# Kernel optimization log

Hardware: AMD Instinct MI355X
Metric: run time of the kernel (lower is better)

The kernel has to match this reference:

```python
import jax, jax.numpy as jnp
import numpy as np

N_NODES = 100000
N_EDGES = 3200000
N_GRAPHS = 2048
VOCAB = 92
H = 64
N_LAYERS = 3


def setup_inputs() -> dict:
    key = jax.random.key(0)
    ks = jax.random.split(key, 16)
    x = jax.random.randint(ks[0], (N_NODES,), 0, VOCAB)
    edge_index = jax.random.randint(ks[1], (2, N_EDGES), 0, N_NODES)
    batch = jnp.sort(jax.random.randint(ks[2], (N_NODES,), 0, N_GRAPHS))
    s = 0.1
    return {
        "x": x,
        "edge_index": edge_index,
        "batch": batch,
        "emb": jax.random.normal(ks[3], (VOCAB, H), jnp.float32) * s,
        "conv_w": jax.random.normal(ks[4], (N_LAYERS, H, H), jnp.float32) * s,
        "conv_b": jax.random.normal(ks[5], (N_LAYERS, H), jnp.float32) * s,
        "w1": jax.random.normal(ks[6], (H, H // 2), jnp.float32) * s,
        "b1": jax.random.normal(ks[7], (H // 2,), jnp.float32) * s,
        "w2": jax.random.normal(ks[8], (H // 2, H // 4), jnp.float32) * s,
        "b2": jax.random.normal(ks[9], (H // 4,), jnp.float32) * s,
        "w3": jax.random.normal(ks[10], (H // 4, 1), jnp.float32) * s,
        "b3": jax.random.normal(ks[11], (1,), jnp.float32) * s,
    }


def _gcn_graph(edge_index, n_nodes):
    # add self-loops, then symmetric degree normalization (PyG GCNConv default)
    loop = jnp.arange(n_nodes)
    row = jnp.concatenate([edge_index[0], loop])  # source
    col = jnp.concatenate([edge_index[1], loop])  # target (aggregation index)
    deg = jnp.zeros((n_nodes,), jnp.float32).at[col].add(1.0)
    dinv = jnp.where(deg > 0, jax.lax.rsqrt(deg), 0.0)
    norm = dinv[row] * dinv[col]  # [E+N]
    return row, col, norm


def _forward(x, edge_index, batch, emb, conv_w, conv_b, w1, b1, w2, b2, w3, b3):
    n = x.shape[0]
    row, col, norm = _gcn_graph(edge_index, n)
    h = emb[x]  # [N,H] embedding lookup
    for i in range(N_LAYERS):
        t = h @ conv_w[i]  # linear transform first (GCNConv)
        msg = t[row] * norm[:, None]  # gather + edge scaling
        agg = jax.ops.segment_sum(msg, col, num_segments=n)  # scatter-add
        h_new = jax.nn.relu(agg + conv_b[i])
        h = h_new if i == 0 else h + h_new  # residual after first layer
    # global mean pool over graphs
    sums = jax.ops.segment_sum(h, batch, num_segments=N_GRAPHS)
    cnt = jax.ops.segment_sum(jnp.ones((n,), h.dtype), batch, num_segments=N_GRAPHS)
    g = sums / jnp.maximum(cnt, 1.0)[:, None]  # [G,H]
    # predictor MLP (dropout is identity in eval)
    g = jax.nn.relu(g @ w1 + b1)
    g = jax.nn.relu(g @ w2 + b2)
    return g @ w3 + b3  # [G,1]


def reference(x, edge_index, batch, emb, conv_w, conv_b, w1, b1, w2, b2, w3, b3):
    return _forward(x, edge_index, batch, emb, conv_w, conv_b, w1, b1, w2, b2, w3, b3)
```

## Files before the change

kernel.cpp:

```cpp
#include <hip/hip_runtime.h>

#define N_NODES 100000
#define N_EDGES 3200000
#define N_GRAPHS 2048
#define VOCAB 92
#define H 64
#define N_LAYERS 3

#define BUCK_BITS 6
#define BUCK_NODES (1 << BUCK_BITS)
#define NBUCK ((N_NODES + BUCK_NODES - 1) / BUCK_NODES)

#define PART_BLOCKS 256
#define EDGES_PER_PART (N_EDGES / PART_BLOCKS)
#define BS_STRIDE (NBUCK + 1)

#define BIN_CAP 2560

#define G0_TILE 64
#define SBINS_STRIDE 100
#define SB_STRIDE 104

#define FL_TILE 64
#define A_STRIDE 72

typedef _Float16 half8 __attribute__((ext_vector_type(8)));
typedef _Float16 half2t __attribute__((ext_vector_type(2)));
typedef float f32x4 __attribute__((ext_vector_type(4)));

__device__ inline unsigned short f2bf(float f) {
    union { float f; unsigned u; } v; v.f = f;
    unsigned u = v.u;
    u += 0x7fffu + ((u >> 16) & 1u);
    return (unsigned short)(u >> 16);
}
__device__ inline float bfhi(unsigned p) {
    union { unsigned u; float f; } v; v.u = p & 0xffff0000u; return v.f;
}
__device__ inline float bflo(unsigned p) {
    union { unsigned u; float f; } v; v.u = p << 16; return v.f;
}
__device__ inline float bf2f(unsigned short b) {
    union { unsigned u; float f; } v; v.u = ((unsigned)b) << 16; return v.f;
}


__device__ inline unsigned char fp8e(float v) {
    union { float f; unsigned u; } a; a.f = v + 0.015625f;
    unsigned u = a.u + 0x0007FFFFu + ((a.u >> 20) & 1u);
    return (unsigned char)((u >> 20) - 960u);
}

__device__ inline half2t ph(unsigned u) {
    union { unsigned u; half2t h; } t; t.u = u; return t.h;
}
__device__ inline unsigned hu(half2t h) {
    union { half2t h; unsigned u; } t; t.h = h; return t.u;
}

__device__ inline void unpack_add8(uint2 v, half2t* a) {
    a[0] += ph(((v.x & 0x00FF00FFu) << 7) + 0x20002000u);
    a[1] += ph(((v.x >> 1) & 0x7F807F80u) + 0x20002000u);
    a[2] += ph(((v.y & 0x00FF00FFu) << 7) + 0x20002000u);
    a[3] += ph(((v.y >> 1) & 0x7F807F80u) + 0x20002000u);
}


__global__ void k_pre(const float* __restrict__ emb, const float* __restrict__ W0,
                      float* __restrict__ M, int* __restrict__ bcnt,
                      int* __restrict__ srpad) {
    int v = blockIdx.x, c = threadIdx.x;
    int i = v * 64 + c;
    if (i < NBUCK) bcnt[i] = 0;
    if (v == 0 && c < 64) srpad[c] = 0;
    float acc = 0.0f;
#pragma unroll
    for (int k = 0; k < H; ++k) acc += emb[v * H + k] * W0[k * H + c];
    M[v * H + c] = acc;
}

__global__ __launch_bounds__(1024) void k_binA(const int* __restrict__ row,
                                               const int* __restrict__ col,
                                               int* __restrict__ bcnt,
                                               int* __restrict__ blkstart,
                                               int* __restrict__ staging) {
    __shared__ int lh[NBUCK];
    __shared__ int lsc[NBUCK];
    __shared__ int s[2048];
    int tid = threadIdx.x;
    int base = blockIdx.x * EDGES_PER_PART;

    for (int i = tid; i < NBUCK; i += 1024) lh[i] = 0;
    __syncthreads();
    for (int k = tid; k < EDGES_PER_PART; k += 1024)
        atomicAdd(&lh[col[base + k] >> BUCK_BITS], 1);
    __syncthreads();

    int p0 = tid, p1 = tid + 1024;
    int v0 = (p0 < NBUCK) ? lh[p0] : 0;
    int v1 = (p1 < NBUCK) ? lh[p1] : 0;
    s[p0] = v0; s[p1] = v1;
    __syncthreads();
    for (int off = 1; off < 2048; off <<= 1) {
        int t0 = (p0 >= off) ? s[p0 - off] : 0;
        int t1 = (p1 >= off) ? s[p1 - off] : 0;
        __syncthreads();
        s[p0] += t0; s[p1] += t1;
        __syncthreads();
    }
    int* myrow = blkstart + (size_t)blockIdx.x * BS_STRIDE;
    if (p0 < NBUCK) {
        int e = s[p0] - v0;
        lsc[p0] = e;
        myrow[p0] = base + e;
        if (v0) atomicAdd(&bcnt[p0], v0);
        lh[p0] = 0;
    }
    if (p1 < NBUCK) {
        int e = s[p1] - v1;
        lsc[p1] = e;
        myrow[p1] = base + e;
        if (v1) atomicAdd(&bcnt[p1], v1);
        lh[p1] = 0;
    }
    if (tid == 0) myrow[NBUCK] = base + EDGES_PER_PART;
    __syncthreads();

    for (int k = tid; k < EDGES_PER_PART; k += 1024) {
        int c = col[base + k];
        int b = c >> BUCK_BITS;
        int r = atomicAdd(&lh[b], 1);
        staging[base + lsc[b] + r] = row[base + k] | ((c & (BUCK_NODES - 1)) << 17);
    }
}

__global__ void k_bscan(const int* __restrict__ bcnt, int* __restrict__ bbase) {
    __shared__ int s[2048];
    int tid = threadIdx.x;
    int p0 = tid, p1 = tid + 1024;
    int v0 = (p0 < NBUCK) ? bcnt[p0] : 0;
    int v1 = (p1 < NBUCK) ? bcnt[p1] : 0;
    s[p0] = v0; s[p1] = v1;
    __syncthreads();
    for (int off = 1; off < 2048; off <<= 1) {
        int t0 = (p0 >= off) ? s[p0 - off] : 0;
        int t1 = (p1 >= off) ? s[p1 - off] : 0;
        __syncthreads();
        s[p0] += t0; s[p1] += t1;
        __syncthreads();
    }
    if (p0 < NBUCK) bbase[p0] = s[p0] - v0;
    if (p1 < NBUCK) bbase[p1] = s[p1] - v1;
    if (tid == 0) bbase[NBUCK] = N_EDGES;
}

__global__ __launch_bounds__(256) void k_binB(const int* __restrict__ staging,
                                              const int* __restrict__ blkstart,
                                              const int* __restrict__ bbase,
                                              const int* __restrict__ x,
                                              int* __restrict__ sorted_e,
                                              int* __restrict__ degi,
                                              int* __restrict__ row_start,
                                              float* __restrict__ dinv,
                                              unsigned* __restrict__ packed) {
    __shared__ int lde[BUCK_NODES];
    __shared__ int lsc[BUCK_NODES];
    __shared__ int sl[BIN_CAP];
    __shared__ int s2[PART_BLOCKS];
    int b = blockIdx.x, tid = threadIdx.x;
    int n0 = b << BUCK_BITS;
    int s0 = bbase[b], s1 = bbase[b + 1];
    int total = s1 - s0;
    bool fit = (total <= BIN_CAP);

    const int* brow = blkstart + (size_t)tid * BS_STRIDE;
    int st = brow[b];
    int cnt = brow[b + 1] - st;

    if (tid < BUCK_NODES) lde[tid] = 0;
    s2[tid] = cnt;
    __syncthreads();
    for (int off = 1; off < PART_BLOCKS; off <<= 1) {
        int v = (tid >= off) ? s2[tid - off] : 0;
        __syncthreads();
        s2[tid] += v;
        __syncthreads();
    }
    int excl = s2[tid] - cnt;

    if (fit) {
        for (int i = 0; i < cnt; ++i) {
            int p = staging[st + i];
            sl[excl + i] = p;
            atomicAdd(&lde[p >> 17], 1);
        }
    } else {
        for (int i = 0; i < cnt; ++i)
            atomicAdd(&lde[staging[st + i] >> 17], 1);
    }
    __syncthreads();

    if (tid < BUCK_NODES) lsc[tid] = lde[tid];
    __syncthreads();
    for (int off = 1; off < BUCK_NODES; off <<= 1) {
        int v = (tid >= off && tid < BUCK_NODES) ? lsc[tid - off] : 0;
        __syncthreads();
        if (tid < BUCK_NODES) lsc[tid] += v;
        __syncthreads();
    }
    if (tid < BUCK_NODES) {
        int n = n0 + tid;
        int ex = lsc[tid] - lde[tid];
        if (n < N_NODES) {
            row_start[n] = s0 + ex;
            degi[n] = lde[tid];
            float dv = rsqrtf((float)(lde[tid] + 1));
            dinv[n] = dv;
            packed[n] = ((unsigned)f2bf(dv) << 16) | (unsigned)x[n];
        }
        lsc[tid] = ex;
        lde[tid] = 0;
    }
    __syncthreads();
    if (fit) {
        for (int i = tid; i < total; i += 256) {
            int p = sl[i];
            int ln = p >> 17;
            int r = atomicAdd(&lde[ln], 1);
            sorted_e[s0 + lsc[ln] + r] = p;
        }
    } else {
        for (int i = 0; i < cnt; ++i) {
            int p = staging[st + i];
            int ln = p >> 17;
            int r = atomicAdd(&lde[ln], 1);
            sorted_e[s0 + lsc[ln] + r] = p;
        }
    }
}

__global__ __launch_bounds__(256) void k_gather0_mfma(
    const int* __restrict__ sorted_e, const int* __restrict__ bbase,
    const unsigned* __restrict__ packed,
    const float* __restrict__ M, const float* __restrict__ dinv,
    const float* __restrict__ bias, unsigned short* __restrict__ h,
    unsigned char* __restrict__ qout) {
    __shared__ float Sbins[G0_TILE][SBINS_STRIDE];
    __shared__ _Float16 Sb[G0_TILE][SB_STRIDE];
    __shared__ _Float16 Blds[H][SB_STRIDE];

    int tid = threadIdx.x;
    int b = blockIdx.x;
    int n0 = b << BUCK_BITS;

    for (int i = tid; i < G0_TILE * SBINS_STRIDE; i += 256)
        ((float*)Sbins)[i] = 0.0f;
    {
        int c = tid & 63, v0 = tid >> 6;
        for (int v = v0; v < VOCAB; v += 4)
            Blds[c][v] = (_Float16)M[v * H + c];
        Blds[c][VOCAB + v0] = (_Float16)0.0f;
    }
    __syncthreads();

    if (tid < G0_TILE) {
        int n = n0 + tid;
        if (n < N_NODES) {
            unsigned p = packed[n];
            atomicAdd(&Sbins[tid][p & 127u], __uint_as_float(p & 0xffff0000u));
        }
    }
    {
        int s0 = bbase[b], s1 = bbase[b + 1];
        int i = s0 + tid;
        for (; i + 256 < s1; i += 512) {
            int p0 = sorted_e[i];
            int p1 = sorted_e[i + 256];
            unsigned k0 = packed[p0 & 0x1FFFF];
            unsigned k1 = packed[p1 & 0x1FFFF];
            atomicAdd(&Sbins[p0 >> 17][k0 & 127u], __uint_as_float(k0 & 0xffff0000u));
            atomicAdd(&Sbins[p1 >> 17][k1 & 127u], __uint_as_float(k1 & 0xffff0000u));
        }
        if (i < s1) {
            int p0 = sorted_e[i];
            unsigned k0 = packed[p0 & 0x1FFFF];
            atomicAdd(&Sbins[p0 >> 17][k0 & 127u], __uint_as_float(k0 & 0xffff0000u));
        }
    }
    __syncthreads();

    {
        int r0 = tid >> 2, k0 = (tid & 3) * 24;
#pragma unroll
        for (int m = 0; m < 3; ++m) {
            f32x4 f0 = *(const f32x4*)&Sbins[r0][k0 + 8 * m];
            f32x4 f1 = *(const f32x4*)&Sbins[r0][k0 + 8 * m + 4];
            half8 o;
            o[0] = (_Float16)f0[0]; o[1] = (_Float16)f0[1];
            o[2] = (_Float16)f0[2]; o[3] = (_Float16)f0[3];
            o[4] = (_Float16)f1[0]; o[5] = (_Float16)f1[1];
            o[6] = (_Float16)f1[2]; o[7] = (_Float16)f1[3];
            *(half8*)&Sb[r0][k0 + 8 * m] = o;
        }
    }
    __syncthreads();

    int w = tid >> 6, lane = tid & 63;
    int l15 = lane & 15, l4 = lane >> 4;
    half8 afr[3];
#pragma unroll
    for (int ks = 0; ks < 3; ++ks)
        afr[ks] = *(const half8*)&Sb[(w << 4) + l15][ks * 32 + l4 * 8];

    f32x4 acc[4];
#pragma unroll
    for (int c = 0; c < 4; ++c) {
        f32x4 a = {0.0f, 0.0f, 0.0f, 0.0f};
#pragma unroll
        for (int ks = 0; ks < 3; ++ks) {
            half8 bfr = *(const half8*)&Blds[c * 16 + l15][ks * 32 + l4 * 8];
            a = __builtin_amdgcn_mfma_f32_16x16x32_f16(afr[ks], bfr, a, 0, 0, 0);
        }
        acc[c] = a;
    }

    int rbase = (w << 4) + l4 * 4;
    float di4[4];
#pragma unroll
    for (int r = 0; r < 4; ++r) {
        int n = n0 + rbase + r;
        di4[r] = (n < N_NODES) ? dinv[n] : 0.0f;
    }
#pragma unroll
    for (int c = 0; c < 4; ++c) {
        float bb = bias[c * 16 + l15];
#pragma unroll
        for (int r = 0; r < 4; ++r) {
            int n = n0 + rbase + r;
            if (n < N_NODES) {
                float v = fmaxf(acc[c][r] * di4[r] + bb, 0.0f);
                h[(size_t)n * H + c * 16 + l15] = f2bf(v);
                qout[(size_t)n * H + c * 16 + l15] = fp8e(16.0f * di4[r] * v);
            }
        }
    }
}

__global__ __launch_bounds__(512) void k_fused(
    const int* __restrict__ sorted_e, const int* __restrict__ row_start,
    const int* __restrict__ degi, const unsigned char* __restrict__ q,
    const float* __restrict__ dinv, const float* __restrict__ W,
    const float* __restrict__ bias, unsigned short* __restrict__ h,
    unsigned char* __restrict__ qout, int last) {
    __shared__ _Float16 Alds[FL_TILE][A_STRIDE];
    __shared__ _Float16 Blds[H][A_STRIDE];

    int tid = threadIdx.x;
    int n0 = blockIdx.x * FL_TILE;

    {
        int c = tid & 63, k0 = (tid >> 6) * 8;
#pragma unroll
        for (int k = 0; k < 8; ++k)
            Blds[c][k0 + k] = (_Float16)W[(k0 + k) * H + c];
    }

    int w = tid >> 6, lane = tid & 63;
    int s = lane >> 3;
    int j = lane & 7;
    const uint2* q2 = (const uint2*)q;

    for (int ni = 0; ni < 8; ++ni) {
        int nl = (w << 3) + ni;
        int n = n0 + nl;
        int d = 0, st = 0;
        if (n < N_NODES) { d = degi[n]; st = row_start[n]; }
        const int* srp = sorted_e + st;
        half2t a[4];
#pragma unroll
        for (int k = 0; k < 4; ++k) a[k] = ph(0u);

        int srA = srp[s];
        int srB = srp[8 + s];
        int e = 0;
        for (; e + 16 <= d; e += 16) {
            uint2 va = q2[(size_t)(srA & 0x1FFFF) * 8 + j];
            uint2 vb = q2[(size_t)(srB & 0x1FFFF) * 8 + j];
            srA = srp[e + 16 + s];
            srB = srp[e + 24 + s];
            unpack_add8(va, a);
            unpack_add8(vb, a);
        }
        if (e < d) {
            uint2 va = q2[(size_t)(srA & 0x1FFFF) * 8 + j];
            uint2 vb = q2[(size_t)(srB & 0x1FFFF) * 8 + j];
            if (e + s >= d) { va.x = 0x08080808u; va.y = 0x08080808u; }
            if (e + 8 + s >= d) { vb.x = 0x08080808u; vb.y = 0x08080808u; }
            unpack_add8(va, a);
            unpack_add8(vb, a);
        }
#pragma unroll
        for (int k = 0; k < 4; ++k) a[k] += ph(__shfl_xor(hu(a[k]), 8, 64));
#pragma unroll
        for (int k = 0; k < 4; ++k) a[k] += ph(__shfl_xor(hu(a[k]), 16, 64));
#pragma unroll
        for (int k = 0; k < 4; ++k) a[k] += ph(__shfl_xor(hu(a[k]), 32, 64));
        if (s == 0) {
            half8 o;
            if (n < N_NODES) {
                uint2 vs = q2[(size_t)n * 8 + j];
                unpack_add8(vs, a);
                int nch = (d + 15) >> 4;
                _Float16 corr = (_Float16)((float)(16 * nch + 1) * 0.015625f);
                half2t c2 = {corr, corr};
                half2t e0 = a[0] - c2, o0 = a[1] - c2;
                half2t e1 = a[2] - c2, o1 = a[3] - c2;
                o[0] = e0[0]; o[1] = o0[0]; o[2] = e0[1]; o[3] = o0[1];
                o[4] = e1[0]; o[5] = o1[0]; o[6] = e1[1]; o[7] = o1[1];
            } else {
#pragma unroll
                for (int k = 0; k < 8; ++k) o[k] = (_Float16)0.0f;
            }
            *(half8*)&Alds[nl][j * 8] = o;
        }
    }
    __syncthreads();

    int l15 = lane & 15, l4 = lane >> 4;
    int rw = (w & 3) << 4;
    int cb = (w >> 2) << 1;
    half8 afr[2];
#pragma unroll
    for (int ks = 0; ks < 2; ++ks)
        afr[ks] = *(const half8*)&Alds[rw + l15][ks * 32 + l4 * 8];

    f32x4 acc[2];
#pragma unroll
    for (int ci = 0; ci < 2; ++ci) {
        f32x4 a = {0.0f, 0.0f, 0.0f, 0.0f};
#pragma unroll
        for (int ks = 0; ks < 2; ++ks) {
            half8 bfr = *(const half8*)&Blds[(cb + ci) * 16 + l15][ks * 32 + l4 * 8];
            a = __builtin_amdgcn_mfma_f32_16x16x32_f16(afr[ks], bfr, a, 0, 0, 0);
        }
        acc[ci] = a;
    }

    int rbase = rw + l4 * 4;
    float di4[4];
#pragma unroll
    for (int r = 0; r < 4; ++r) {
        int n = n0 + rbase + r;
        di4[r] = (n < N_NODES) ? dinv[n] : 0.0f;
    }
#pragma unroll
    for (int ci = 0; ci < 2; ++ci) {
        float bb = bias[(cb + ci) * 16 + l15];
#pragma unroll
        for (int r = 0; r < 4; ++r) {
            int n = n0 + rbase + r;
            if (n < N_NODES) {
                size_t idx = (size_t)n * H + (cb + ci) * 16 + l15;
                float v = bf2f(h[idx]) +
                          fmaxf(acc[ci][r] * (di4[r] * 0.0625f) + bb, 0.0f);
                h[idx] = f2bf(v);
                if (!last) qout[idx] = fp8e(16.0f * di4[r] * v);
            }
        }
    }
}

__global__ __launch_bounds__(256) void k_poolmlp(
    const unsigned short* __restrict__ h, const int* __restrict__ batch,
    const float* __restrict__ w1, const float* __restrict__ b1,
    const float* __restrict__ w2, const float* __restrict__ b2,
    const float* __restrict__ w3, const float* __restrict__ b3,
    float* __restrict__ out) {
    __shared__ float2 part[8][32];
    __shared__ float sg[H];
    __shared__ float s1[32];
    __shared__ float s2[16];
    int g = blockIdx.x, tid = threadIdx.x;
    int lo = 0, hi = N_NODES;
    while (lo < hi) { int mid = (lo + hi) >> 1; if (batch[mid] < g) lo = mid + 1; else hi = mid; }
    int lo2 = lo, hi2 = N_NODES;
    while (lo2 < hi2) { int mid = (lo2 + hi2) >> 1; if (batch[mid] < g + 1) lo2 = mid + 1; else hi2 = mid; }

    int hw = tid >> 5;
    int c = tid & 31;
    const unsigned* h2 = (const unsigned*)h;
    float ax = 0.0f, ay = 0.0f;
    for (int n = lo + hw; n < lo2; n += 8) {
        unsigned u = h2[(size_t)n * 32 + c];
        ax += bflo(u); ay += bfhi(u);
    }
    part[hw][c] = make_float2(ax, ay);
    __syncthreads();
    if (tid < 32) {
        float sx = 0.0f, sy = 0.0f;
#pragma unroll
        for (int k = 0; k < 8; ++k) { sx += part[k][tid].x; sy += part[k][tid].y; }
        float cntf = fmaxf((float)(lo2 - lo), 1.0f);
        sg[2 * tid] = sx / cntf;
        sg[2 * tid + 1] = sy / cntf;
    }
    __syncthreads();
    if (tid < 32) {
        float a = b1[tid];
#pragma unroll
        for (int k = 0; k < H; ++k) a += sg[k] * w1[k * 32 + tid];
        s1[tid] = fmaxf(a, 0.0f);
    }
    __syncthreads();
    if (tid < 16) {
        float a = b2[tid];
#pragma unroll
        for (int k = 0; k < 32; ++k) a += s1[k] * w2[k * 16 + tid];
        s2[tid] = fmaxf(a, 0.0f);
    }
    __syncthreads();
    if (tid == 0) {
        float a = b3[0];
#pragma unroll
        for (int k = 0; k < 16; ++k) a += s2[k] * w3[k];
        out[g] = a;
    }
}


extern "C" void kernel_launch(void* const* d_in, const int* in_sizes, int n_in,
                              void* d_out, int out_size, void* d_ws, size_t ws_size,
                              hipStream_t stream) {
    const int*   x      = (const int*)d_in[0];
    const int*   eidx   = (const int*)d_in[1];
    const int*   batch  = (const int*)d_in[2];
    const float* emb    = (const float*)d_in[3];
    const float* conv_w = (const float*)d_in[4];
    const float* conv_b = (const float*)d_in[5];
    const float* w1     = (const float*)d_in[6];
    const float* b1     = (const float*)d_in[7];
    const float* w2     = (const float*)d_in[8];
    const float* b2     = (const float*)d_in[9];
    const float* w3     = (const float*)d_in[10];
    const float* b3     = (const float*)d_in[11];
    float* out = (float*)d_out;

    const int* row = eidx;
    const int* col = eidx + N_EDGES;

    char* wsb = (char*)d_ws;
    size_t off = 0;
    auto alloc = [&](size_t elems) { void* p = wsb + off; off += ((elems * 4 + 255) & ~(size_t)255); return p; };
    int*      bcnt       = (int*)alloc(NBUCK);
    int*      bbase      = (int*)alloc(NBUCK + 1);
    int*      blkstart   = (int*)alloc((size_t)PART_BLOCKS * BS_STRIDE);
    int*      row_start  = (int*)alloc(N_NODES);
    int*      degi       = (int*)alloc(N_NODES);
    float*    dinv       = (float*)alloc(N_NODES);
    unsigned* packed     = (unsigned*)alloc(N_NODES);
    float*    M          = (float*)alloc(VOCAB * H);
    int*      sorted_e   = (int*)alloc(N_EDGES + 64);
    unsigned short* h    = (unsigned short*)alloc((size_t)N_NODES * H / 2);
    unsigned char* qa    = (unsigned char*)alloc((size_t)N_EDGES);
    unsigned char* qb    = (unsigned char*)alloc((size_t)N_NODES * H / 4);

    int* staging = (int*)qa;

    const int B = 256;
    const int gF = (N_NODES + FL_TILE - 1) / FL_TILE;

    hipLaunchKernelGGL(k_pre, dim3(VOCAB), dim3(H), 0, stream,
                       emb, conv_w, M, bcnt, sorted_e + N_EDGES);
    hipLaunchKernelGGL(k_binA, dim3(PART_BLOCKS), dim3(1024), 0, stream,
                       row, col, bcnt, blkstart, staging);
    hipLaunchKernelGGL(k_bscan, dim3(1), dim3(1024), 0, stream, bcnt, bbase);
    hipLaunchKernelGGL(k_binB, dim3(NBUCK), dim3(256), 0, stream, staging, blkstart,
                       bbase, x, sorted_e, degi, row_start, dinv, packed);

    hipLaunchKernelGGL(k_gather0_mfma, dim3(NBUCK), dim3(B), 0, stream,
                       sorted_e, bbase, packed, M, dinv, conv_b, h, qb);

    hipLaunchKernelGGL(k_fused, dim3(gF), dim3(512), 0, stream,
                       sorted_e, row_start, degi, qb, dinv,
                       conv_w + (size_t)1 * H * H, conv_b + 1 * H, h, qa, 0);
    hipLaunchKernelGGL(k_fused, dim3(gF), dim3(512), 0, stream,
                       sorted_e, row_start, degi, qa, dinv,
                       conv_w + (size_t)2 * H * H, conv_b + 2 * H, h, qb, 1);

    hipLaunchKernelGGL(k_poolmlp, dim3(N_GRAPHS), dim3(256), 0, stream,
                       h, batch, w1, b1, w2, b2, w3, b3, out);

    (void)in_sizes; (void)n_in; (void)out_size; (void)ws_size;
}
```

Measured before the change: 324.6 us.

## Fuse bin sort with layer-0 gather and compute degrees in partition pass

Per-node degrees are now counted with global atomics during the first partition pass, and a small kernel derives dinv and the packed key from them. This removes the need for the second binning kernel to produce degrees before anything else can use them. That second binning kernel is merged into the layer-0 gather, so sorted edges feed the histogram accumulation directly instead of being written and re-read. The fused layer gather loop is also unrolled to four neighbour loads per iteration, with the padding correction adjusted to match. The cost is 3.2M global atomics on the degree array and a larger, more LDS-heavy fused kernel, which may reduce occupancy.

```diff
diff --git a/kernel.cpp b/kernel.cpp
--- a/kernel.cpp
+++ b/kernel.cpp
@@ -68,11 +68,12 @@
 
 __global__ void k_pre(const float* __restrict__ emb, const float* __restrict__ W0,
                       float* __restrict__ M, int* __restrict__ bcnt,
-                      int* __restrict__ srpad) {
+                      int* __restrict__ srpad, int* __restrict__ degi) {
     int v = blockIdx.x, c = threadIdx.x;
     int i = v * 64 + c;
     if (i < NBUCK) bcnt[i] = 0;
     if (v == 0 && c < 64) srpad[c] = 0;
+    for (int t = i; t < N_NODES; t += VOCAB * 64) degi[t] = 0;
     float acc = 0.0f;
 #pragma unroll
     for (int k = 0; k < H; ++k) acc += emb[v * H + k] * W0[k * H + c];
@@ -83,7 +84,8 @@
                                                const int* __restrict__ col,
                                                int* __restrict__ bcnt,
                                                int* __restrict__ blkstart,
-                                               int* __restrict__ staging) {
+                                               int* __restrict__ staging,
+                                               int* __restrict__ degi) {
     __shared__ int lh[NBUCK];
     __shared__ int lsc[NBUCK];
     __shared__ int s[2048];
@@ -92,8 +94,11 @@
 
     for (int i = tid; i < NBUCK; i += 1024) lh[i] = 0;
     __syncthreads();
-    for (int k = tid; k < EDGES_PER_PART; k += 1024)
-        atomicAdd(&lh[col[base + k] >> BUCK_BITS], 1);
+    for (int k = tid; k < EDGES_PER_PART; k += 1024) {
+        int c = col[base + k];
+        atomicAdd(&lh[c >> BUCK_BITS], 1);
+        atomicAdd(&degi[c], 1);
+    }
     __syncthreads();
 
     int p0 = tid, p1 = tid + 1024;
@@ -134,6 +139,16 @@
     }
 }
 
+__global__ void k_meta(const int* __restrict__ degi, const int* __restrict__ x,
+                       float* __restrict__ dinv, unsigned* __restrict__ packed) {
+    int n = blockIdx.x * 256 + threadIdx.x;
+    if (n < N_NODES) {
+        float dv = rsqrtf((float)(degi[n] + 1));
+        dinv[n] = dv;
+        packed[n] = ((unsigned)f2bf(dv) << 16) | (unsigned)x[n];
+    }
+}
+
 __global__ void k_bscan(const int* __restrict__ bcnt, int* __restrict__ bbase) {
     __shared__ int s[2048];
     int tid = threadIdx.x;
@@ -154,104 +169,26 @@
     if (tid == 0) bbase[NBUCK] = N_EDGES;
 }
 
-__global__ __launch_bounds__(256) void k_binB(const int* __restrict__ staging,
-                                              const int* __restrict__ blkstart,
-                                              const int* __restrict__ bbase,
-                                              const int* __restrict__ x,
-                                              int* __restrict__ sorted_e,
-                                              int* __restrict__ degi,
-                                              int* __restrict__ row_start,
-                                              float* __restrict__ dinv,
-                                              unsigned* __restrict__ packed) {
+__global__ __launch_bounds__(256) void k_bg(
+    const int* __restrict__ staging, const int* __restrict__ blkstart,
+    const int* __restrict__ bbase, const int* __restrict__ degi,
+    const unsigned* __restrict__ packed, const float* __restrict__ M,
+    const float* __restrict__ dinv, const float* __restrict__ bias,
+    int* __restrict__ sorted_e, int* __restrict__ row_start,
+    unsigned short* __restrict__ h, unsigned char* __restrict__ qout) {
     __shared__ int lde[BUCK_NODES];
     __shared__ int lsc[BUCK_NODES];
+    __shared__ int s2[PART_BLOCKS];
     __shared__ int sl[BIN_CAP];
-    __shared__ int s2[PART_BLOCKS];
-    int b = blockIdx.x, tid = threadIdx.x;
-    int n0 = b << BUCK_BITS;
-    int s0 = bbase[b], s1 = bbase[b + 1];
-    int total = s1 - s0;
-    bool fit = (total <= BIN_CAP);
-
-    const int* brow = blkstart + (size_t)tid * BS_STRIDE;
-    int st = brow[b];
-    int cnt = brow[b + 1] - st;
-
-    if (tid < BUCK_NODES) lde[tid] = 0;
-    s2[tid] = cnt;
-    __syncthreads();
-    for (int off = 1; off < PART_BLOCKS; off <<= 1) {
-        int v = (tid >= off) ? s2[tid - off] : 0;
-        __syncthreads();
-        s2[tid] += v;
-        __syncthreads();
-    }
-    int excl = s2[tid] - cnt;
-
-    if (fit) {
-        for (int i = 0; i < cnt; ++i) {
-            int p = staging[st + i];
-            sl[excl + i] = p;
-            atomicAdd(&lde[p >> 17], 1);
-        }
-    } else {
-        for (int i = 0; i < cnt; ++i)
-            atomicAdd(&lde[staging[st + i] >> 17], 1);
-    }
-    __syncthreads();
-
-    if (tid < BUCK_NODES) lsc[tid] = lde[tid];
-    __syncthreads();
-    for (int off = 1; off < BUCK_NODES; off <<= 1) {
-        int v = (tid >= off && tid < BUCK_NODES) ? lsc[tid - off] : 0;
-        __syncthreads();
-        if (tid < BUCK_NODES) lsc[tid] += v;
-        __syncthreads();
-    }
-    if (tid < BUCK_NODES) {
-        int n = n0 + tid;
-        int ex = lsc[tid] - lde[tid];
-        if (n < N_NODES) {
-            row_start[n] = s0 + ex;
-            degi[n] = lde[tid];
-            float dv = rsqrtf((float)(lde[tid] + 1));
-            dinv[n] = dv;
-            packed[n] = ((unsigned)f2bf(dv) << 16) | (unsigned)x[n];
-        }
-        lsc[tid] = ex;
-        lde[tid] = 0;
-    }
-    __syncthreads();
-    if (fit) {
-        for (int i = tid; i < total; i += 256) {
-            int p = sl[i];
-            int ln = p >> 17;
-            int r = atomicAdd(&lde[ln], 1);
-            sorted_e[s0 + lsc[ln] + r] = p;
-        }
-    } else {
-        for (int i = 0; i < cnt; ++i) {
-            int p = staging[st + i];
-            int ln = p >> 17;
-            int r = atomicAdd(&lde[ln], 1);
-            sorted_e[s0 + lsc[ln] + r] = p;
-        }
-    }
-}
-
-__global__ __launch_bounds__(256) void k_gather0_mfma(
-    const int* __restrict__ sorted_e, const int* __restrict__ bbase,
-    const unsigned* __restrict__ packed,
-    const float* __restrict__ M, const float* __restrict__ dinv,
-    const float* __restrict__ bias, unsigned short* __restrict__ h,
-    unsigned char* __restrict__ qout) {
     __shared__ float Sbins[G0_TILE][SBINS_STRIDE];
     __shared__ _Float16 Sb[G0_TILE][SB_STRIDE];
     __shared__ _Float16 Blds[H][SB_STRIDE];
 
-    int tid = threadIdx.x;
-    int b = blockIdx.x;
+    int b = blockIdx.x, tid = threadIdx.x;
     int n0 = b << BUCK_BITS;
+    int s0 = bbase[b], s1v = bbase[b + 1];
+    int total = s1v - s0;
+    bool fit = (total <= BIN_CAP);
 
     for (int i = tid; i < G0_TILE * SBINS_STRIDE; i += 256)
         ((float*)Sbins)[i] = 0.0f;
@@ -261,6 +198,41 @@
             Blds[c][v] = (_Float16)M[v * H + c];
         Blds[c][VOCAB + v0] = (_Float16)0.0f;
     }
+
+    const int* brow = blkstart + (size_t)tid * BS_STRIDE;
+    int st = brow[b];
+    int cnt = brow[b + 1] - st;
+    s2[tid] = cnt;
+    if (tid < BUCK_NODES) {
+        int n = n0 + tid;
+        lde[tid] = (n < N_NODES) ? degi[n] : 0;
+    }
+    __syncthreads();
+    for (int off = 1; off < PART_BLOCKS; off <<= 1) {
+        int v = (tid >= off) ? s2[tid - off] : 0;
+        __syncthreads();
+        s2[tid] += v;
+        __syncthreads();
+    }
+    int excl2 = s2[tid] - cnt;
+    if (tid < BUCK_NODES) lsc[tid] = lde[tid];
+    __syncthreads();
+    for (int off = 1; off < BUCK_NODES; off <<= 1) {
+        int v = (tid >= off && tid < BUCK_NODES) ? lsc[tid - off] : 0;
+        __syncthreads();
+        if (tid < BUCK_NODES) lsc[tid] += v;
+        __syncthreads();
+    }
+    if (tid < BUCK_NODES) {
+        int n = n0 + tid;
+        int ex = lsc[tid] - lde[tid];
+        if (n < N_NODES) row_start[n] = s0 + ex;
+        lsc[tid] = ex;
+        lde[tid] = 0;
+    }
+    if (fit) {
+        for (int i = 0; i < cnt; ++i) sl[excl2 + i] = staging[st + i];
+    }
     __syncthreads();
 
     if (tid < G0_TILE) {
@@ -270,21 +242,23 @@
             atomicAdd(&Sbins[tid][p & 127u], __uint_as_float(p & 0xffff0000u));
         }
     }
-    {
-        int s0 = bbase[b], s1 = bbase[b + 1];
-        int i = s0 + tid;
-        for (; i + 256 < s1; i += 512) {
-            int p0 = sorted_e[i];
-            int p1 = sorted_e[i + 256];
-            unsigned k0 = packed[p0 & 0x1FFFF];
-            unsigned k1 = packed[p1 & 0x1FFFF];
-            atomicAdd(&Sbins[p0 >> 17][k0 & 127u], __uint_as_float(k0 & 0xffff0000u));
-            atomicAdd(&Sbins[p1 >> 17][k1 & 127u], __uint_as_float(k1 & 0xffff0000u));
-        }
-        if (i < s1) {
-            int p0 = sorted_e[i];
-            unsigned k0 = packed[p0 & 0x1FFFF];
-            atomicAdd(&Sbins[p0 >> 17][k0 & 127u], __uint_as_float(k0 & 0xffff0000u));
+    if (fit) {
+        for (int i = tid; i < total; i += 256) {
+            int p = sl[i];
+            int ln = p >> 17;
+            int r = atomicAdd(&lde[ln], 1);
+            sorted_e[s0 + lsc[ln] + r] = p;
+            unsigned k = packed[p & 0x1FFFF];
+            atomicAdd(&Sbins[ln][k & 127u], __uint_as_float(k & 0xffff0000u));
+        }
+    } else {
+        for (int i = 0; i < cnt; ++i) {
+            int p = staging[st + i];
+            int ln = p >> 17;
+            int r = atomicAdd(&lde[ln], 1);
+            sorted_e[s0 + lsc[ln] + r] = p;
+            unsigned k = packed[p & 0x1FFFF];
+            atomicAdd(&Sbins[ln][k & 127u], __uint_as_float(k & 0xffff0000u));
         }
     }
     __syncthreads();
@@ -380,24 +354,29 @@
 #pragma unroll
         for (int k = 0; k < 4; ++k) a[k] = ph(0u);
 
-        int srA = srp[s];
-        int srB = srp[8 + s];
+        int sr0 = srp[s], sr1 = srp[8 + s], sr2 = srp[16 + s], sr3 = srp[24 + s];
         int e = 0;
-        for (; e + 16 <= d; e += 16) {
-            uint2 va = q2[(size_t)(srA & 0x1FFFF) * 8 + j];
-            uint2 vb = q2[(size_t)(srB & 0x1FFFF) * 8 + j];
-            srA = srp[e + 16 + s];
-            srB = srp[e + 24 + s];
-            unpack_add8(va, a);
-            unpack_add8(vb, a);
+        for (; e + 32 <= d; e += 32) {
+            uint2 v0 = q2[(size_t)(sr0 & 0x1FFFF) * 8 + j];
+            uint2 v1 = q2[(size_t)(sr1 & 0x1FFFF) * 8 + j];
+            uint2 v2 = q2[(size_t)(sr2 & 0x1FFFF) * 8 + j];
+            uint2 v3 = q2[(size_t)(sr3 & 0x1FFFF) * 8 + j];
+            sr0 = srp[e + 32 + s]; sr1 = srp[e + 40 + s];
+            sr2 = srp[e + 48 + s]; sr3 = srp[e + 56 + s];
+            unpack_add8(v0, a); unpack_add8(v1, a);
+            unpack_add8(v2, a); unpack_add8(v3, a);
         }
         if (e < d) {
-            uint2 va = q2[(size_t)(srA & 0x1FFFF) * 8 + j];
-            uint2 vb = q2[(size_t)(srB & 0x1FFFF) * 8 + j];
-            if (e + s >= d) { va.x = 0x08080808u; va.y = 0x08080808u; }
-            if (e + 8 + s >= d) { vb.x = 0x08080808u; vb.y = 0x08080808u; }
-            unpack_add8(va, a);
-            unpack_add8(vb, a);
+            uint2 v0 = q2[(size_t)(sr0 & 0x1FFFF) * 8 + j];
+            uint2 v1 = q2[(size_t)(sr1 & 0x1FFFF) * 8 + j];
+            uint2 v2 = q2[(size_t)(sr2 & 0x1FFFF) * 8 + j];
+            uint2 v3 = q2[(size_t)(sr3 & 0x1FFFF) * 8 + j];
+            if (e + s >= d)      { v0.x = 0x08080808u; v0.y = 0x08080808u; }
+            if (e + 8 + s >= d)  { v1.x = 0x08080808u; v1.y = 0x08080808u; }
+            if (e + 16 + s >= d) { v2.x = 0x08080808u; v2.y = 0x08080808u; }
+            if (e + 24 + s >= d) { v3.x = 0x08080808u; v3.y = 0x08080808u; }
+            unpack_add8(v0, a); unpack_add8(v1, a);
+            unpack_add8(v2, a); unpack_add8(v3, a);
         }
 #pragma unroll
         for (int k = 0; k < 4; ++k) a[k] += ph(__shfl_xor(hu(a[k]), 8, 64));
@@ -410,8 +389,8 @@
             if (n < N_NODES) {
                 uint2 vs = q2[(size_t)n * 8 + j];
                 unpack_add8(vs, a);
-                int nch = (d + 15) >> 4;
-                _Float16 corr = (_Float16)((float)(16 * nch + 1) * 0.015625f);
+                int nch = (d + 31) >> 5;
+                _Float16 corr = (_Float16)((float)(32 * nch + 1) * 0.015625f);
                 half2t c2 = {corr, corr};
                 half2t e0 = a[0] - c2, o0 = a[1] - c2;
                 half2t e1 = a[2] - c2, o1 = a[3] - c2;
@@ -566,19 +545,19 @@
 
     int* staging = (int*)qa;
 
-    const int B = 256;
     const int gF = (N_NODES + FL_TILE - 1) / FL_TILE;
 
     hipLaunchKernelGGL(k_pre, dim3(VOCAB), dim3(H), 0, stream,
-                       emb, conv_w, M, bcnt, sorted_e + N_EDGES);
+                       emb, conv_w, M, bcnt, sorted_e + N_EDGES, degi);
     hipLaunchKernelGGL(k_binA, dim3(PART_BLOCKS), dim3(1024), 0, stream,
-                       row, col, bcnt, blkstart, staging);
+                       row, col, bcnt, blkstart, staging, degi);
+    hipLaunchKernelGGL(k_meta, dim3((N_NODES + 255) / 256), dim3(256), 0, stream,
+                       degi, x, dinv, packed);
     hipLaunchKernelGGL(k_bscan, dim3(1), dim3(1024), 0, stream, bcnt, bbase);
-    hipLaunchKernelGGL(k_binB, dim3(NBUCK), dim3(256), 0, stream, staging, blkstart,
-                       bbase, x, sorted_e, degi, row_start, dinv, packed);
-
-    hipLaunchKernelGGL(k_gather0_mfma, dim3(NBUCK), dim3(B), 0, stream,
-                       sorted_e, bbase, packed, M, dinv, conv_b, h, qb);
+
+    hipLaunchKernelGGL(k_bg, dim3(NBUCK), dim3(256), 0, stream,
+                       staging, blkstart, bbase, degi, packed, M, dinv, conv_b,
+                       sorted_e, row_start, h, qb);
 
     hipLaunchKernelGGL(k_fused, dim3(gF), dim3(512), 0, stream,
                        sorted_e, row_start, degi, qb, dinv,
```

After: 453.2 us. 39.6% more time.
